# Performance work log

Measured on AMD Instinct MI355X. Metric: run time of the kernel, lower is better.

The kernel has to match this reference:

```python
import jax, jax.numpy as jnp
import numpy as np

NUM_HEADS = 8
STRIDE = 1
PAD = 1


def _conv(x, w, stride=STRIDE, pad=PAD):
    return jax.lax.conv_general_dilated(
        x, w, (stride, stride), [(pad, pad), (pad, pad)],
        dimension_numbers=("NCHW", "OIHW", "NCHW"))


def setup_inputs() -> dict:
    key = jax.random.key(0)
    ks = jax.random.split(key, 5)
    B, C, H, W = 8, 64, 56, 56
    nh = NUM_HEADS
    x = jax.random.normal(ks[0], (B, C, H, W), dtype=jnp.float32)
    # Conv weights, small init for numerical stability
    Wq = jax.random.normal(ks[1], (C * nh, C, 3, 3), dtype=jnp.float32) * 0.05
    Wk = jax.random.normal(ks[2], (C * nh, C, 3, 3), dtype=jnp.float32) * 0.05
    Wv = jax.random.normal(ks[3], (C * nh, C, 3, 3), dtype=jnp.float32) * 0.05
    Wu = jax.random.normal(ks[4], (C, C * nh, 1, 1), dtype=jnp.float32) * 0.05
    return {"x": x, "Wq": Wq, "Wk": Wk, "Wv": Wv, "Wu": Wu}


def reference(x, Wq, Wk, Wv, Wu):
    B, C, H, W = x.shape
    nh = NUM_HEADS
    # projections: [B, nh*C, H, W] -> [B, nh, C, H, W] -> [B, C, nh, H, W]
    def proj(w):
        y = _conv(x, w).reshape(B, nh, C, H, W)
        return jnp.transpose(y, (0, 2, 1, 3, 4))
    q = proj(Wq)  # [B, C, nh, H, W]
    k = proj(Wk)
    v = proj(Wv)
    scale = 1.0 / np.sqrt(C * nh).astype(np.float32)
    # contract over heads axis ('n'), attend over channel axis: [B, Cq, H, W, Ck]
    scores = jnp.einsum("bqnhw,bknhw->bqhwk", q, k) * scale
    attn = jax.nn.softmax(scores, axis=-1)
    # attended: [B, Cq, nh, H, W]
    attended = jnp.einsum("bqhwk,bknhw->bqnhw", attn, v)
    out = _conv(attended.reshape(B, C * nh, H, W), Wu, stride=1, pad=0)
    return jax.nn.relu(out)
```

## Files before the change

kernel.cpp:

```cpp
#include <hip/hip_runtime.h>
#include <hip/hip_bf16.h>

#define HW   56
#define CIN  64
#define OC   512
#define NPIX (HW * HW)
#define PEL  ((size_t)8 * NPIX * OC)

typedef unsigned short ushort_t;
typedef __attribute__((ext_vector_type(8))) short short8;
typedef __attribute__((ext_vector_type(4))) float floatx4;
typedef __attribute__((ext_vector_type(16))) float floatx16;

static __device__ __forceinline__ ushort_t f2bf(float f) {
  __hip_bfloat16 h = __float2bfloat16(f);
  return *(ushort_t*)&h;
}

__global__ __launch_bounds__(256)
void prep_kernel(const float* __restrict__ x, const float* __restrict__ W0,
                 const float* __restrict__ W1, const float* __restrict__ W2,
                 const float* __restrict__ Wu, ushort_t* __restrict__ xT,
                 ushort_t* __restrict__ Wb, ushort_t* __restrict__ WuP) {
  __shared__ ushort_t lx[CIN * HW];
  const int bid = blockIdx.x;
  const int tid = threadIdx.x;

  if (bid < 448) {
    const int h = bid % HW, b = bid / HW;
    for (int idx = tid; idx < CIN * HW; idx += 256) {
      int c = idx / HW, w = idx - c * HW;
      lx[idx] = f2bf(x[((size_t)(b * CIN + c) * HW + h) * HW + w]);
    }
    __syncthreads();
    ushort_t* dst = xT + ((size_t)(b * HW + h)) * HW * CIN;
    for (int i = tid; i < (CIN * HW) / 4; i += 256) {
      int e0 = i * 4;
      int w = e0 >> 6, c0 = e0 & 63;
      ushort4 o;
      o.x = lx[(c0 + 0) * HW + w];
      o.y = lx[(c0 + 1) * HW + w];
      o.z = lx[(c0 + 2) * HW + w];
      o.w = lx[(c0 + 3) * HW + w];
      ((ushort4*)dst)[i] = o;
    }
  } else if (bid < 832) {
    const int u = bid - 448;
    const int sel = u / 128;
    const int j = (u % 128) * 4 + (tid >> 6);
    const int cin = tid & 63;
    const float* W = sel == 0 ? W0 : (sel == 1 ? W1 : W2);
    ushort_t* Ds = Wb + (size_t)sel * 9 * OC * CIN;
    const int src = (sel < 2) ? ((j & 7) * 64 + (j >> 3)) : j;
    #pragma unroll
    for (int tap = 0; tap < 9; ++tap)
      Ds[((size_t)tap * OC + j) * CIN + cin] = f2bf(W[(size_t)src * 576 + cin * 9 + tap]);
  } else {
    const int el = (bid - 832) * 256 + tid;
    WuP[el] = f2bf(Wu[el]);
  }
}

#define XLS 72
#define XROW (58 * XLS)

__global__ __launch_bounds__(256, 2)
void conv3x3_qkv(const ushort_t* __restrict__ xT, const ushort_t* __restrict__ Wb,
                 ushort_t* __restrict__ yq) {
  __shared__ __align__(16) ushort_t xl[6 * XROW];

  const int tid  = threadIdx.x;
  const int lane = tid & 63;
  const int wv   = tid >> 6;
  const int g    = blockIdx.x;
  const int ob   = blockIdx.y;
  const int b    = blockIdx.z & 7;
  const int s    = blockIdx.z >> 3;
  const int h0   = g * 4;
  const int l31  = lane & 31;
  const int khi  = lane >> 5;

  int rowcol[7], wwv[7];
  #pragma unroll
  for (int t = 0; t < 7; ++t) {
    int p = t * 32 + l31;
    int row = p / HW, ww = p - row * HW;
    rowcol[t] = (row * 58 + ww) * XLS;
    wwv[t] = ww;
  }

  const ushort_t* wb0 = Wb + (size_t)s * 9 * OC * CIN +
                        ((size_t)(ob * 128 + wv * 32 + l31)) * CIN + khi * 8;

  for (int r = 0; r < 6; ++r) {
    int gh = h0 - 1 + r;
    if (gh >= 0 && gh < HW) {
      const uint4* src = (const uint4*)(xT + ((size_t)(b * HW + gh) * HW) * CIN);
      for (int idx = tid; idx < 448; idx += 256) {
        int w = idx >> 3, c8 = idx & 7;
        int col = 1 + w;
        int p8 = (c8 + 2 * ((col >> 3) & 3)) & 7;
        *(uint4*)&xl[(r * 58 + col) * XLS + p8 * 8] = src[idx];
      }
      if (tid < 16) {
        int col = (tid >> 3) ? 57 : 0, c8 = tid & 7;
        int p8 = (c8 + 2 * ((col >> 3) & 3)) & 7;
        *(uint4*)&xl[(r * 58 + col) * XLS + p8 * 8] = (uint4){0, 0, 0, 0};
      }
    } else {
      for (int idx = tid; idx < 464; idx += 256) {
        int col = idx >> 3, c8 = idx & 7;
        int p8 = (c8 + 2 * ((col >> 3) & 3)) & 7;
        *(uint4*)&xl[(r * 58 + col) * XLS + p8 * 8] = (uint4){0, 0, 0, 0};
      }
    }
  }

  short8 Bf[2][4];
  #pragma unroll
  for (int ck = 0; ck < 4; ++ck)
    Bf[0][ck] = *(const short8*)(wb0 + ck * 16);

  floatx16 acc[7];
  #pragma unroll
  for (int t = 0; t < 7; ++t) acc[t] = (floatx16)(0.0f);

  __syncthreads();

  #pragma unroll
  for (int tap = 0; tap < 9; ++tap) {
    const int p = tap & 1;
    if (tap < 8) {
      #pragma unroll
      for (int ck = 0; ck < 4; ++ck)
        Bf[p ^ 1][ck] = *(const short8*)(wb0 + (size_t)(tap + 1) * OC * CIN + ck * 16);
    }
    const int kh = tap / 3, kw = tap - kh * 3;
    int baddr[7], b8[7];
    #pragma unroll
    for (int t = 0; t < 7; ++t) {
      int j = wwv[t] + kw;
      baddr[t] = rowcol[t] + (kh * 58 + kw) * XLS;
      b8[t] = khi + 2 * ((j >> 3) & 3);
    }
    #pragma unroll
    for (int ck = 0; ck < 4; ++ck) {
      #pragma unroll
      for (int t = 0; t < 7; ++t) {
        int chunk = (b8[t] + 2 * ck) & 7;
        short8 af = *(const short8*)&xl[baddr[t] + chunk * 8];
        acc[t] = __builtin_amdgcn_mfma_f32_32x32x16_bf16(af, Bf[p][ck], acc[t], 0, 0, 0);
      }
    }
  }

  ushort_t* y = yq + (size_t)s * PEL;
  const int oc = ob * 128 + wv * 32 + l31;
  #pragma unroll
  for (int t = 0; t < 7; ++t) {
    #pragma unroll
    for (int i = 0; i < 16; ++i) {
      int p = t * 32 + (i & 3) + 8 * (i >> 2) + 4 * khi;
      int row = p / HW, ww = p - row * HW;
      size_t pb = ((size_t)((b * HW + h0 + row) * HW + ww)) * OC;
      y[pb + oc] = f2bf(acc[t][i]);
    }
  }
}

#define PST  72
#define A2ST 520

__global__ __launch_bounds__(256, 3)
void attn_kernel(const ushort_t* __restrict__ q, const ushort_t* __restrict__ k,
                 const ushort_t* __restrict__ v, const ushort_t* __restrict__ WuP,
                 float* __restrict__ out) {
  __shared__ __align__(16) ushort_t Pl[4][64 * PST];
  __shared__ __align__(16) ushort_t a2[16 * A2ST];

  const int tid  = threadIdx.x;
  const int lane = tid & 63;
  const int wv   = tid >> 6;
  const int l15  = lane & 15;
  const int quad = lane >> 4;
  const int p0   = blockIdx.x * 16;
  const int b    = blockIdx.y;
  const size_t ibase = ((size_t)b * NPIX + p0) * 512;

  ushort_t* Pw = &Pl[wv][0];
  const float scale = 0.044194173824159216f;

  auto loadpix = [&](int plocal, short8 qf[4], short8 kf[4], short8 vf[2]) {
    const ushort_t* qp = q + ibase + (size_t)plocal * 512;
    const ushort_t* kp = k + ibase + (size_t)plocal * 512;
    const ushort_t* vp = v + ibase + (size_t)plocal * 512;
    #pragma unroll
    for (int nt = 0; nt < 4; ++nt)
      qf[nt] = *(const short8*)(qp + (nt * 16 + l15) * 8);
    #pragma unroll
    for (int mt = 0; mt < 4; ++mt) {
      kf[mt] = (short8){0, 0, 0, 0, 0, 0, 0, 0};
      if (quad == 0) kf[mt] = *(const short8*)(kp + (mt * 16 + l15) * 8);
    }
    #pragma unroll
    for (int ck = 0; ck < 2; ++ck)
      vf[ck] = *(const short8*)(vp + (l15 & 7) * 64 + ck * 32 + quad * 8);
  };

  short8 qf[4], kf[4], vf[2];
  loadpix(wv * 4, qf, kf, vf);

  #pragma unroll
  for (int i = 0; i < 4; ++i) {
    const int plocal = wv * 4 + i;
    short8 qn[4], kn[4], vn[2];
    if (i < 3) loadpix(plocal + 1, qn, kn, vn);

    floatx4 S[4][4];
    #pragma unroll
    for (int mt = 0; mt < 4; ++mt)
      #pragma unroll
      for (int nt = 0; nt < 4; ++nt) S[mt][nt] = (floatx4){0.f, 0.f, 0.f, 0.f};
    #pragma unroll
    for (int mt = 0; mt < 4; ++mt)
      #pragma unroll
      for (int nt = 0; nt < 4; ++nt)
        S[mt][nt] = __builtin_amdgcn_mfma_f32_16x16x32_bf16(kf[mt], qf[nt], S[mt][nt], 0, 0, 0);

    #pragma unroll
    for (int nt = 0; nt < 4; ++nt) {
      float m = S[0][nt][0];
      #pragma unroll
      for (int mt = 0; mt < 4; ++mt)
        #pragma unroll
        for (int r = 0; r < 4; ++r) m = fmaxf(m, S[mt][nt][r]);
      m = fmaxf(m, __shfl_xor(m, 16));
      m = fmaxf(m, __shfl_xor(m, 32));
      float sum = 0.f;
      #pragma unroll
      for (int mt = 0; mt < 4; ++mt)
        #pragma unroll
        for (int r = 0; r < 4; ++r) {
          float e = __expf((S[mt][nt][r] - m) * scale);
          S[mt][nt][r] = e;
          sum += e;
        }
      sum += __shfl_xor(sum, 16);
      sum += __shfl_xor(sum, 32);
      float inv = __builtin_amdgcn_rcpf(sum);
      #pragma unroll
      for (int mt = 0; mt < 4; ++mt) {
        ushort4 w4;
        w4.x = f2bf(S[mt][nt][0] * inv);
        w4.y = f2bf(S[mt][nt][1] * inv);
        w4.z = f2bf(S[mt][nt][2] * inv);
        w4.w = f2bf(S[mt][nt][3] * inv);
        *(ushort4*)&Pw[(nt * 16 + l15) * PST + mt * 16 + quad * 4] = w4;
      }
    }

    floatx4 T[4];
    #pragma unroll
    for (int nt = 0; nt < 4; ++nt) T[nt] = (floatx4){0.f, 0.f, 0.f, 0.f};
    #pragma unroll
    for (int ck = 0; ck < 2; ++ck) {
      #pragma unroll
      for (int nt = 0; nt < 4; ++nt) {
        short8 pf = *(const short8*)&Pw[(nt * 16 + l15) * PST + ck * 32 + quad * 8];
        T[nt] = __builtin_amdgcn_mfma_f32_16x16x32_bf16(vf[ck], pf, T[nt], 0, 0, 0);
      }
    }
    if (quad < 2) {
      #pragma unroll
      for (int nt = 0; nt < 4; ++nt) {
        ushort4 w4;
        w4.x = f2bf(T[nt][0]);
        w4.y = f2bf(T[nt][1]);
        w4.z = f2bf(T[nt][2]);
        w4.w = f2bf(T[nt][3]);
        *(ushort4*)&a2[plocal * A2ST + (nt * 16 + l15) * 8 + quad * 4] = w4;
      }
    }

    if (i < 3) {
      #pragma unroll
      for (int z = 0; z < 4; ++z) { qf[z] = qn[z]; kf[z] = kn[z]; }
      vf[0] = vn[0];
      vf[1] = vn[1];
    }
  }
  __syncthreads();

  floatx4 O = (floatx4){0.f, 0.f, 0.f, 0.f};
  #pragma unroll
  for (int ck = 0; ck < 16; ++ck) {
    short8 aw = *(const short8*)(WuP + (size_t)(wv * 16 + l15) * 512 + ck * 32 + quad * 8);
    short8 bw = *(const short8*)&a2[l15 * A2ST + ck * 32 + quad * 8];
    O = __builtin_amdgcn_mfma_f32_16x16x32_bf16(aw, bw, O, 0, 0, 0);
  }
  #pragma unroll
  for (int r = 0; r < 4; ++r) {
    int co = wv * 16 + quad * 4 + r;
    out[((size_t)b * 64 + co) * NPIX + p0 + l15] = fmaxf(O[r], 0.f);
  }
}

extern "C" void kernel_launch(void* const* d_in, const int* in_sizes, int n_in,
                              void* d_out, int out_size, void* d_ws, size_t ws_size,
                              hipStream_t stream) {
  const float* x  = (const float*)d_in[0];
  const float* Wq = (const float*)d_in[1];
  const float* Wk = (const float*)d_in[2];
  const float* Wv = (const float*)d_in[3];
  const float* Wu = (const float*)d_in[4];
  float* out = (float*)d_out;

  const size_t xT_elems = (size_t)8 * NPIX * CIN;
  const size_t w_elems  = (size_t)9 * OC * CIN;
  const size_t wu_elems = (size_t)64 * 512;
  ushort_t* xT  = (ushort_t*)d_ws;
  ushort_t* Wb  = xT + xT_elems;
  ushort_t* WuP = Wb + 3 * w_elems;
  ushort_t* q   = WuP + wu_elems;
  ushort_t* k   = q + PEL;
  ushort_t* v   = k + PEL;

  prep_kernel<<<960, 256, 0, stream>>>(x, Wq, Wk, Wv, Wu, xT, Wb, WuP);

  dim3 cgrid(14, 4, 24);
  conv3x3_qkv<<<cgrid, 256, 0, stream>>>(xT, Wb, q);

  attn_kernel<<<dim3(NPIX / 16, 8), 256, 0, stream>>>(q, k, v, WuP, out);
}
```

Measured before the change: 173.4 us.

## Reuse staged input tile across q/k/v projections in one conv block

Each conv block now loops over the three projection weights (q, k, v) while the 6-row input tile stays in LDS, so the grid shrinks from 24 to 8 in z and the input staging is done once instead of three times. The weight prefetch is now a rolling single-step register buffer that runs across the projection boundary. The LDS swizzle is changed to depend on row instead of column. The trade-off is a third of the blocks (448 total, fewer waves to fill the GPU) and a longer serial loop per block.

```diff
diff --git a/kernel.cpp b/kernel.cpp
--- a/kernel.cpp
+++ b/kernel.cpp
@@ -74,96 +74,99 @@
   const int wv   = tid >> 6;
   const int g    = blockIdx.x;
   const int ob   = blockIdx.y;
-  const int b    = blockIdx.z & 7;
-  const int s    = blockIdx.z >> 3;
+  const int b    = blockIdx.z;
   const int h0   = g * 4;
   const int l31  = lane & 31;
   const int khi  = lane >> 5;
 
-  int rowcol[7], wwv[7];
+  int rowcol[7], rowv[7];
   #pragma unroll
   for (int t = 0; t < 7; ++t) {
     int p = t * 32 + l31;
     int row = p / HW, ww = p - row * HW;
     rowcol[t] = (row * 58 + ww) * XLS;
-    wwv[t] = ww;
-  }
-
-  const ushort_t* wb0 = Wb + (size_t)s * 9 * OC * CIN +
-                        ((size_t)(ob * 128 + wv * 32 + l31)) * CIN + khi * 8;
+    rowv[t] = row;
+  }
+
+  const ushort_t* wb0 = Wb + ((size_t)(ob * 128 + wv * 32 + l31)) * CIN + khi * 8;
 
   for (int r = 0; r < 6; ++r) {
     int gh = h0 - 1 + r;
+    const int sw = 2 * ((-r) & 3);
     if (gh >= 0 && gh < HW) {
       const uint4* src = (const uint4*)(xT + ((size_t)(b * HW + gh) * HW) * CIN);
       for (int idx = tid; idx < 448; idx += 256) {
         int w = idx >> 3, c8 = idx & 7;
         int col = 1 + w;
-        int p8 = (c8 + 2 * ((col >> 3) & 3)) & 7;
+        int p8 = (c8 + sw) & 7;
         *(uint4*)&xl[(r * 58 + col) * XLS + p8 * 8] = src[idx];
       }
       if (tid < 16) {
         int col = (tid >> 3) ? 57 : 0, c8 = tid & 7;
-        int p8 = (c8 + 2 * ((col >> 3) & 3)) & 7;
+        int p8 = (c8 + sw) & 7;
         *(uint4*)&xl[(r * 58 + col) * XLS + p8 * 8] = (uint4){0, 0, 0, 0};
       }
     } else {
       for (int idx = tid; idx < 464; idx += 256) {
         int col = idx >> 3, c8 = idx & 7;
-        int p8 = (c8 + 2 * ((col >> 3) & 3)) & 7;
+        int p8 = (c8 + sw) & 7;
         *(uint4*)&xl[(r * 58 + col) * XLS + p8 * 8] = (uint4){0, 0, 0, 0};
       }
     }
   }
 
-  short8 Bf[2][4];
+  short8 BfA[4], BfB[4];
   #pragma unroll
   for (int ck = 0; ck < 4; ++ck)
-    Bf[0][ck] = *(const short8*)(wb0 + ck * 16);
-
-  floatx16 acc[7];
-  #pragma unroll
-  for (int t = 0; t < 7; ++t) acc[t] = (floatx16)(0.0f);
+    BfA[ck] = *(const short8*)(wb0 + ck * 16);
 
   __syncthreads();
 
-  #pragma unroll
-  for (int tap = 0; tap < 9; ++tap) {
-    const int p = tap & 1;
-    if (tap < 8) {
-      #pragma unroll
-      for (int ck = 0; ck < 4; ++ck)
-        Bf[p ^ 1][ck] = *(const short8*)(wb0 + (size_t)(tap + 1) * OC * CIN + ck * 16);
-    }
-    const int kh = tap / 3, kw = tap - kh * 3;
-    int baddr[7], b8[7];
+  #pragma unroll 1
+  for (int s = 0; s < 3; ++s) {
+    floatx16 acc[7];
+    #pragma unroll
+    for (int t = 0; t < 7; ++t) acc[t] = (floatx16)(0.0f);
+
+    #pragma unroll
+    for (int tap = 0; tap < 9; ++tap) {
+      const int wtap = s * 9 + tap;
+      if (wtap < 26) {
+        #pragma unroll
+        for (int ck = 0; ck < 4; ++ck)
+          BfB[ck] = *(const short8*)(wb0 + (size_t)(wtap + 1) * (OC * CIN) + ck * 16);
+      }
+      const int kh = tap / 3, kw = tap - kh * 3;
+      int baddr[7], b8[7];
+      #pragma unroll
+      for (int t = 0; t < 7; ++t) {
+        baddr[t] = rowcol[t] + (kh * 58 + kw) * XLS;
+        b8[t] = khi + 2 * ((-(rowv[t] + kh)) & 3);
+      }
+      #pragma unroll
+      for (int ck = 0; ck < 4; ++ck) {
+        #pragma unroll
+        for (int t = 0; t < 7; ++t) {
+          int chunk = (b8[t] + 2 * ck) & 7;
+          short8 af = *(const short8*)&xl[baddr[t] + chunk * 8];
+          acc[t] = __builtin_amdgcn_mfma_f32_32x32x16_bf16(af, BfA[ck], acc[t], 0, 0, 0);
+        }
+      }
+      #pragma unroll
+      for (int ck = 0; ck < 4; ++ck) BfA[ck] = BfB[ck];
+    }
+
+    ushort_t* y = yq + (size_t)s * PEL;
+    const int oc = ob * 128 + wv * 32 + l31;
     #pragma unroll
     for (int t = 0; t < 7; ++t) {
-      int j = wwv[t] + kw;
-      baddr[t] = rowcol[t] + (kh * 58 + kw) * XLS;
-      b8[t] = khi + 2 * ((j >> 3) & 3);
-    }
-    #pragma unroll
-    for (int ck = 0; ck < 4; ++ck) {
-      #pragma unroll
-      for (int t = 0; t < 7; ++t) {
-        int chunk = (b8[t] + 2 * ck) & 7;
-        short8 af = *(const short8*)&xl[baddr[t] + chunk * 8];
-        acc[t] = __builtin_amdgcn_mfma_f32_32x32x16_bf16(af, Bf[p][ck], acc[t], 0, 0, 0);
-      }
-    }
-  }
-
-  ushort_t* y = yq + (size_t)s * PEL;
-  const int oc = ob * 128 + wv * 32 + l31;
-  #pragma unroll
-  for (int t = 0; t < 7; ++t) {
-    #pragma unroll
-    for (int i = 0; i < 16; ++i) {
-      int p = t * 32 + (i & 3) + 8 * (i >> 2) + 4 * khi;
-      int row = p / HW, ww = p - row * HW;
-      size_t pb = ((size_t)((b * HW + h0 + row) * HW + ww)) * OC;
-      y[pb + oc] = f2bf(acc[t][i]);
+      #pragma unroll
+      for (int i = 0; i < 16; ++i) {
+        int p = t * 32 + (i & 3) + 8 * (i >> 2) + 4 * khi;
+        int row = p / HW, ww = p - row * HW;
+        size_t pb = ((size_t)((b * HW + h0 + row) * HW + ww)) * OC;
+        y[pb + oc] = f2bf(acc[t][i]);
+      }
     }
   }
 }
@@ -327,7 +330,7 @@
 
   prep_kernel<<<960, 256, 0, stream>>>(x, Wq, Wk, Wv, Wu, xT, Wb, WuP);
 
-  dim3 cgrid(14, 4, 24);
+  dim3 cgrid(14, 4, 8);
   conv3x3_qkv<<<cgrid, 256, 0, stream>>>(xT, Wb, q);
 
   attn_kernel<<<dim3(NPIX / 16, 8), 256, 0, stream>>>(q, k, v, WuP, out);
```

Measured after the change: 159.6 us. 8.0% less time.
